# Kernel optimization log

Measured on AMD Instinct MI355X. Metric: run time of the kernel, lower is better.

## Reference

```python
import jax, jax.numpy as jnp
import numpy as np

B, T, C = 2, 512, 128
H = 4 * C
EPS_LN = 1e-5
EPS_WKV = 1e-6


def setup_inputs() -> dict:
    key = jax.random.key(0)
    ks = jax.random.split(key, 12)
    def rn(i, shape, s):
        return jax.random.normal(ks[i], shape, jnp.float32) * s
    return {
        "x": jax.random.normal(ks[0], (B, T, C), jnp.float32),
        "ln1_g": jnp.ones((C,), jnp.float32), "ln1_b": jnp.zeros((C,), jnp.float32),
        "mu": rn(1, (C,), 0.1),
        "Wr": rn(2, (C, C), 0.02), "br": jnp.zeros((C,), jnp.float32),
        "Wk": rn(3, (C, C), 0.02), "bk": jnp.zeros((C,), jnp.float32),
        "Wv": rn(4, (C, C), 0.02), "bv": jnp.zeros((C,), jnp.float32),
        "w_decay": rn(5, (C,), 0.5),
        "Wo": rn(6, (C, C), 0.02), "bo": jnp.zeros((C,), jnp.float32),
        "ln2_g": jnp.ones((C,), jnp.float32), "ln2_b": jnp.zeros((C,), jnp.float32),
        "W1": rn(7, (C, H), 0.02), "b1": jnp.zeros((H,), jnp.float32),
        "W2": rn(8, (H, C), 0.02), "b2": jnp.zeros((C,), jnp.float32),
    }


def _ln(x, g, b):
    m = x.mean(-1, keepdims=True)
    v = ((x - m) ** 2).mean(-1, keepdims=True)
    return (x - m) * jax.lax.rsqrt(v + EPS_LN) * g + b


def _wkv_dir(k, v, w_lc):
    # k, v: (B,T,C); w_lc: (T,C) per-(position,channel) decay weight
    p = k[:, :, None, :] * w_lc[None, None, :, :]              # (B,T,L,C)
    p = jnp.exp(p - jax.lax.stop_gradient(p.max(-1, keepdims=True)))  # stable, max over C (as in source, dim=-1)
    p = p / (p.sum(-1, keepdims=True) + EPS_WKV)               # normalize over channel dim, as written in torch
    return jnp.einsum('btlc,blc->btc', p, v)


def _forward(x, ln1_g, ln1_b, mu, Wr, br, Wk, bk, Wv, bv, w_decay, Wo, bo, ln2_g, ln2_b, W1, b1, W2, b2):
    Tn = x.shape[1]
    h = _ln(x, ln1_g, ln1_b)
    # TemporalShift: past half shifted right, future half shifted left
    xp, xf = jnp.split(h, 2, axis=-1)
    xp = jnp.pad(xp, ((0, 0), (1, 0), (0, 0)))[:, :-1]
    xf = jnp.pad(xf, ((0, 0), (0, 1), (0, 0)))[:, 1:]
    hs = h + mu * jnp.concatenate([xp, xf], axis=-1)
    r = jax.nn.sigmoid(hs @ Wr + br)
    k = hs @ Wk + bk
    v = hs @ Wv + bv
    t = jnp.arange(Tn, dtype=x.dtype)[:, None]                 # (T,1)
    neg_w = -jnp.exp(w_decay)[None, :]                         # (1,C)
    w_f = neg_w * (Tn - 1 - t) / (Tn - 1)                      # (T,C)
    w_b = neg_w * t / (Tn - 1)                                 # (T,C)
    x_f = _wkv_dir(k, v, w_f)
    x_b = jnp.flip(_wkv_dir(jnp.flip(k, 1), jnp.flip(v, 1), w_b), 1)
    wk = r * (x_f + x_b) * 0.5
    y = x + wk @ Wo + bo
    h2 = _ln(y, ln2_g, ln2_b)
    m = jax.nn.gelu(h2 @ W1 + b1, approximate=False) @ W2 + b2
    return y + m


def reference(x, ln1_g, ln1_b, mu, Wr, br, Wk, bk, Wv, bv, w_decay, Wo, bo, ln2_g, ln2_b, W1, b1, W2, b2):
    return _forward(x, ln1_g, ln1_b, mu, Wr, br, Wk, bk, Wv, bv, w_decay, Wo, bo, ln2_g, ln2_b, W1, b1, W2, b2)
```

## Files before the change

kernel.cpp:

```cpp
#include <hip/hip_runtime.h>
#include <hip/hip_bf16.h>

#define Bq 2
#define Tq 512
#define Cq 128
#define Hq 512
#define NROW (Bq*Tq)

__device__ __forceinline__ float bfbits2f(unsigned short u) {
    return __uint_as_float(((unsigned)u) << 16);
}
__device__ __forceinline__ bool detect_f32(const void* sent) {
    return *(const unsigned*)sent == 0x3F800000u;
}
#define LD(p, i) (f32 ? ((const float*)(p))[i] : bfbits2f(((const unsigned short*)(p))[i]))
__device__ __forceinline__ float4 LD4(const void* p, int i, bool f32) {
    if (f32) return ((const float4*)p)[i >> 2];
    ushort4 u = *(const ushort4*)((const unsigned short*)p + i);
    return make_float4(bfbits2f(u.x), bfbits2f(u.y), bfbits2f(u.z), bfbits2f(u.w));
}

__global__ __launch_bounds__(512) void k2_qkv(
    const void* __restrict__ sent,
    const void* __restrict__ x,
    const void* __restrict__ ln1g, const void* __restrict__ ln1b,
    const void* __restrict__ mu,
    const void* __restrict__ Wr, const void* __restrict__ br,
    const void* __restrict__ Wk, const void* __restrict__ bk,
    const void* __restrict__ Wv, const void* __restrict__ bv,
    const void* __restrict__ wdec,
    float* __restrict__ r_out, float* __restrict__ u_out,
    float* __restrict__ v_out)
{
    const bool f32 = detect_f32(sent);
    int R0 = blockIdx.x * 2, tid = threadIdx.x;
    int g = tid >> 7, col = tid & 127;
    int t0 = R0 & (Tq - 1);
    int bbase = R0 - t0;

    __shared__ float h4[4][Cq];
    __shared__ float hs2[2][Cq];
    __shared__ float part[4][6][Cq];
    __shared__ float wred[8][2];

    {
        int t = t0 - 1 + g;
        int tcl = min(max(t, 0), Tq - 1);
        int row = bbase + tcl;
        float xv = LD(x, row * Cq + col);
        float s1 = xv, s2 = xv * xv;
        for (int off = 32; off; off >>= 1) {
            s1 += __shfl_xor(s1, off);
            s2 += __shfl_xor(s2, off);
        }
        int wid = tid >> 6;
        if ((tid & 63) == 0) { wred[wid][0] = s1; wred[wid][1] = s2; }
        __syncthreads();
        float S1 = wred[2 * g][0] + wred[2 * g + 1][0];
        float S2 = wred[2 * g][1] + wred[2 * g + 1][1];
        float m  = S1 * (1.f / Cq);
        float va = S2 * (1.f / Cq) - m * m;
        float rs = rsqrtf(va + 1e-5f);
        h4[g][col] = (xv - m) * rs * LD(ln1g, col) + LD(ln1b, col);
    }
    __syncthreads();

    if (g < 2) {
        int r2 = g, tt = t0 + r2;
        float hv = h4[r2 + 1][col];
        float nb;
        if (col < Cq / 2) nb = (tt > 0)      ? h4[r2][col]     : 0.f;
        else              nb = (tt < Tq - 1) ? h4[r2 + 2][col] : 0.f;
        hs2[r2][col] = hv + LD(mu, col) * nb;
    }
    __syncthreads();

    {
        float ar0 = 0.f, ar1 = 0.f, ak0 = 0.f, ak1 = 0.f, av0 = 0.f, av1 = 0.f;
        int c0 = g * 32;
        for (int cc = c0; cc < c0 + 32; cc += 4) {
            float4 h0 = *(const float4*)&hs2[0][cc];
            float4 h1 = *(const float4*)&hs2[1][cc];
            float wr0 = LD(Wr, (cc + 0) * Cq + col);
            float wr1 = LD(Wr, (cc + 1) * Cq + col);
            float wr2 = LD(Wr, (cc + 2) * Cq + col);
            float wr3 = LD(Wr, (cc + 3) * Cq + col);
            float wk0 = LD(Wk, (cc + 0) * Cq + col);
            float wk1 = LD(Wk, (cc + 1) * Cq + col);
            float wk2 = LD(Wk, (cc + 2) * Cq + col);
            float wk3 = LD(Wk, (cc + 3) * Cq + col);
            float wv0 = LD(Wv, (cc + 0) * Cq + col);
            float wv1 = LD(Wv, (cc + 1) * Cq + col);
            float wv2 = LD(Wv, (cc + 2) * Cq + col);
            float wv3 = LD(Wv, (cc + 3) * Cq + col);
            ar0 += h0.x * wr0; ar1 += h1.x * wr0;
            ak0 += h0.x * wk0; ak1 += h1.x * wk0;
            av0 += h0.x * wv0; av1 += h1.x * wv0;
            ar0 += h0.y * wr1; ar1 += h1.y * wr1;
            ak0 += h0.y * wk1; ak1 += h1.y * wk1;
            av0 += h0.y * wv1; av1 += h1.y * wv1;
            ar0 += h0.z * wr2; ar1 += h1.z * wr2;
            ak0 += h0.z * wk2; ak1 += h1.z * wk2;
            av0 += h0.z * wv2; av1 += h1.z * wv2;
            ar0 += h0.w * wr3; ar1 += h1.w * wr3;
            ak0 += h0.w * wk3; ak1 += h1.w * wk3;
            av0 += h0.w * wv3; av1 += h1.w * wv3;
        }
        part[g][0][col] = ar0; part[g][1][col] = ar1;
        part[g][2][col] = ak0; part[g][3][col] = ak1;
        part[g][4][col] = av0; part[g][5][col] = av1;
    }
    __syncthreads();

    if (g < 3) {
#pragma unroll
        for (int r2 = 0; r2 < 2; ++r2) {
            int m = 2 * g + r2;
            float a = (part[0][m][col] + part[1][m][col])
                    + (part[2][m][col] + part[3][m][col]);
            int row = R0 + r2;
            if (g == 0) {
                float rr = 1.f / (1.f + __expf(-(a + LD(br, col))));
                r_out[row * Cq + col] = rr;
            } else if (g == 1) {
                float wd = LD(wdec, col);
                wd = fminf(fmaxf(wd, -20.f), 20.f);
                float negw = -__expf(wd);
                float uu = (a + LD(bk, col)) * negw;
                uu = fminf(fmaxf(uu, -30.f), 30.f);
                u_out[row * Cq + col] = uu;
            } else {
                v_out[row * Cq + col] = a + LD(bv, col);
            }
        }
    }
}

__global__ __launch_bounds__(512) void k3_wkv(
    const void* __restrict__ sent,
    const float* __restrict__ u_in,
    const float* __restrict__ v_in,
    const float* __restrict__ r_in,
    const void* __restrict__ x,
    const void* __restrict__ Wo, const void* __restrict__ bo,
    float* __restrict__ y_out)
{
    const bool f32 = detect_f32(sent);
    int row = blockIdx.x, tid = threadIdx.x;
    int b = row >> 9;
    __shared__ float u_l[Cq];
    __shared__ float rinv_l[Tq];
    __shared__ float wk_l[Cq];
    __shared__ float part[8][Cq];
    __shared__ float part2[4][Cq];
    if (tid < Cq) u_l[tid] = u_in[row * Cq + tid];
    __syncthreads();

    const float inv511 = 1.f / (float)(Tq - 1);
    {
        int l = tid;
        float a = (float)(Tq - 1 - l) * inv511 * 1.44269504f;
        float s0 = 0.f, s1 = 0.f, s2 = 0.f, s3 = 0.f;
        const float4* u4 = (const float4*)u_l;
        for (int cc = 0; cc < Cq / 4; ++cc) {
            float4 uv = u4[cc];
            s0 += exp2f(a * uv.x);
            s1 += exp2f(a * uv.y);
            s2 += exp2f(a * uv.z);
            s3 += exp2f(a * uv.w);
        }
        rinv_l[l] = 1.f / ((s0 + s1) + (s2 + s3) + 1e-6f);
    }
    __syncthreads();

    {
        int cidx = tid & 63, seg = tid >> 6;
        int c2 = cidx * 2;
        float2 uu = *(const float2*)&u_l[c2];
        float g1x = __expf(uu.x * inv511),      g1y = __expf(uu.y * inv511);
        float g2x = g1x * g1x,                  g2y = g1y * g1y;
        float g3x = g2x * g1x,                  g3y = g2y * g1y;
        float g4x = g2x * g2x,                  g4y = g2y * g2y;
        float jb  = (float)(seg * 64);
        float ex  = __expf(uu.x * jb * inv511), ey = __expf(uu.y * jb * inv511);
        float a0x = 0.f, a0y = 0.f, a1x = 0.f, a1y = 0.f;
        float a2x = 0.f, a2y = 0.f, a3x = 0.f, a3y = 0.f;
        const float2* vb2 = (const float2*)(v_in + (size_t)b * Tq * Cq) + cidx;
        int j0 = seg * 64;
        for (int j = j0; j < j0 + 64; j += 4) {
            int l = (Tq - 1) - j;
            float4 rv = *(const float4*)&rinv_l[l - 3];
            float2 v0 = vb2[(size_t)l * 64];
            float2 v1 = vb2[(size_t)(l - 1) * 64];
            float2 v2 = vb2[(size_t)(l - 2) * 64];
            float2 v3 = vb2[(size_t)(l - 3) * 64];
            a0x += v0.x * (ex * rv.w);          a0y += v0.y * (ey * rv.w);
            a1x += v1.x * ((ex * g1x) * rv.z);  a1y += v1.y * ((ey * g1y) * rv.z);
            a2x += v2.x * ((ex * g2x) * rv.y);  a2y += v2.y * ((ey * g2y) * rv.y);
            a3x += v3.x * ((ex * g3x) * rv.x);  a3y += v3.y * ((ey * g3y) * rv.x);
            ex *= g4x; ey *= g4y;
        }
        float px = (a0x + a1x) + (a2x + a3x);
        float py = (a0y + a1y) + (a2y + a3y);
        *(float2*)&part[seg][c2] = make_float2(px, py);
    }
    __syncthreads();
    if (tid < Cq) {
        float acc = ((part[0][tid] + part[1][tid]) + (part[2][tid] + part[3][tid]))
                  + ((part[4][tid] + part[5][tid]) + (part[6][tid] + part[7][tid]));
        wk_l[tid] = r_in[row * Cq + tid] * acc;
    }
    __syncthreads();

    {
        int seg4 = tid >> 7, c = tid & 127;
        float s = 0.f;
        int c0 = seg4 * 32;
        for (int cc = c0; cc < c0 + 32; cc += 4) {
            float4 wv4 = *(const float4*)&wk_l[cc];
            s += wv4.x * LD(Wo, (cc + 0) * Cq + c);
            s += wv4.y * LD(Wo, (cc + 1) * Cq + c);
            s += wv4.z * LD(Wo, (cc + 2) * Cq + c);
            s += wv4.w * LD(Wo, (cc + 3) * Cq + c);
        }
        part2[seg4][c] = s;
    }
    __syncthreads();
    if (tid < Cq)
        y_out[row * Cq + tid] = LD(x, row * Cq + tid)
            + ((part2[0][tid] + part2[1][tid]) + (part2[2][tid] + part2[3][tid]))
            + LD(bo, tid);
}

__global__ __launch_bounds__(512) void k4_ffn(
    const void* __restrict__ sent,
    const float* __restrict__ y_in,
    const void* __restrict__ lng, const void* __restrict__ lnb,
    const void* __restrict__ W1, const void* __restrict__ b1,
    const void* __restrict__ W2, const void* __restrict__ b2,
    void* __restrict__ out)
{
    const bool f32 = detect_f32(sent);
    int R0 = blockIdx.x * 2, tid = threadIdx.x;
    __shared__ float h2s[2][Cq];
    __shared__ float m1s[2][Hq];
    __shared__ float part1[4][2][Hq];
    __shared__ float part[4][2][Cq];
    __shared__ float wred[8][2];
    int r2 = (tid >> 7) & 1, c = tid & 127;
    float yv = 0.f;
    if (tid < 256) yv = y_in[(R0 + r2) * Cq + c];
    float s1 = yv, s2 = yv * yv;
    for (int off = 32; off; off >>= 1) {
        s1 += __shfl_xor(s1, off);
        s2 += __shfl_xor(s2, off);
    }
    int wid = tid >> 6;
    if ((tid & 63) == 0) { wred[wid][0] = s1; wred[wid][1] = s2; }
    __syncthreads();
    if (tid < 256) {
        int w0 = r2 << 1;
        float S1 = wred[w0][0] + wred[w0 + 1][0];
        float S2 = wred[w0][1] + wred[w0 + 1][1];
        float m  = S1 * (1.f / Cq);
        float va = S2 * (1.f / Cq) - m * m;
        float rs = rsqrtf(va + 1e-5f);
        h2s[r2][c] = (yv - m) * rs * LD(lng, c) + LD(lnb, c);
    }
    __syncthreads();

    {
        int kseg = tid >> 7, j4 = (tid & 127) * 4;
        float a00 = 0.f, a01 = 0.f, a02 = 0.f, a03 = 0.f;
        float a10 = 0.f, a11 = 0.f, a12 = 0.f, a13 = 0.f;
        int c0 = kseg * 32;
        for (int cc = c0; cc < c0 + 32; cc += 4) {
            float4 w0 = LD4(W1, (cc + 0) * Hq + j4, f32);
            float4 w1 = LD4(W1, (cc + 1) * Hq + j4, f32);
            float4 w2 = LD4(W1, (cc + 2) * Hq + j4, f32);
            float4 w3 = LD4(W1, (cc + 3) * Hq + j4, f32);
            float4 h0 = *(const float4*)&h2s[0][cc];
            float4 h1 = *(const float4*)&h2s[1][cc];
            a00 += h0.x * w0.x; a01 += h0.x * w0.y; a02 += h0.x * w0.z; a03 += h0.x * w0.w;
            a10 += h1.x * w0.x; a11 += h1.x * w0.y; a12 += h1.x * w0.z; a13 += h1.x * w0.w;
            a00 += h0.y * w1.x; a01 += h0.y * w1.y; a02 += h0.y * w1.z; a03 += h0.y * w1.w;
            a10 += h1.y * w1.x; a11 += h1.y * w1.y; a12 += h1.y * w1.z; a13 += h1.y * w1.w;
            a00 += h0.z * w2.x; a01 += h0.z * w2.y; a02 += h0.z * w2.z; a03 += h0.z * w2.w;
            a10 += h1.z * w2.x; a11 += h1.z * w2.y; a12 += h1.z * w2.z; a13 += h1.z * w2.w;
            a00 += h0.w * w3.x; a01 += h0.w * w3.y; a02 += h0.w * w3.z; a03 += h0.w * w3.w;
            a10 += h1.w * w3.x; a11 += h1.w * w3.y; a12 += h1.w * w3.z; a13 += h1.w * w3.w;
        }
        *(float4*)&part1[kseg][0][j4] = make_float4(a00, a01, a02, a03);
        *(float4*)&part1[kseg][1][j4] = make_float4(a10, a11, a12, a13);
    }
    __syncthreads();
    {
        int j = tid;
        float bb = LD(b1, j);
        float x0 = ((part1[0][0][j] + part1[1][0][j]) + (part1[2][0][j] + part1[3][0][j])) + bb;
        float x1 = ((part1[0][1][j] + part1[1][1][j]) + (part1[2][1][j] + part1[3][1][j])) + bb;
        m1s[0][j] = 0.5f * x0 * (1.f + erff(x0 * 0.70710678f));
        m1s[1][j] = 0.5f * x1 * (1.f + erff(x1 * 0.70710678f));
    }
    __syncthreads();

    {
        int kseg = tid >> 7;
        int h0 = kseg * 128;
        float a0 = 0.f, a1 = 0.f;
        for (int hh = h0; hh < h0 + 128; hh += 8) {
            float4 ma = *(const float4*)&m1s[0][hh];
            float4 mb = *(const float4*)&m1s[0][hh + 4];
            float4 na = *(const float4*)&m1s[1][hh];
            float4 nb = *(const float4*)&m1s[1][hh + 4];
            float w0 = LD(W2, (hh + 0) * Cq + c);
            float w1 = LD(W2, (hh + 1) * Cq + c);
            float w2 = LD(W2, (hh + 2) * Cq + c);
            float w3 = LD(W2, (hh + 3) * Cq + c);
            float w4 = LD(W2, (hh + 4) * Cq + c);
            float w5 = LD(W2, (hh + 5) * Cq + c);
            float w6 = LD(W2, (hh + 6) * Cq + c);
            float w7 = LD(W2, (hh + 7) * Cq + c);
            a0 += ma.x * w0; a1 += na.x * w0;
            a0 += ma.y * w1; a1 += na.y * w1;
            a0 += ma.z * w2; a1 += na.z * w2;
            a0 += ma.w * w3; a1 += na.w * w3;
            a0 += mb.x * w4; a1 += nb.x * w4;
            a0 += mb.y * w5; a1 += nb.y * w5;
            a0 += mb.z * w6; a1 += nb.z * w6;
            a0 += mb.w * w7; a1 += nb.w * w7;
        }
        part[kseg][0][c] = a0;
        part[kseg][1][c] = a1;
    }
    __syncthreads();
    if (tid < 256) {
        float s = ((part[0][r2][c] + part[1][r2][c]) + (part[2][r2][c] + part[3][r2][c]));
        float val = yv + s + LD(b2, c);
        int idx = (R0 + r2) * Cq + c;
        if (f32) ((float*)out)[idx] = val;
        else     ((__hip_bfloat16*)out)[idx] = __float2bfloat16(val);
    }
}

extern "C" void kernel_launch(void* const* d_in, const int* in_sizes, int n_in,
                              void* d_out, int out_size, void* d_ws, size_t ws_size,
                              hipStream_t stream)
{
    const void* x    = d_in[0];
    const void* ln1g = d_in[1];
    const void* ln1b = d_in[2];
    const void* mu   = d_in[3];
    const void* Wr   = d_in[4];
    const void* br   = d_in[5];
    const void* Wk   = d_in[6];
    const void* bk   = d_in[7];
    const void* Wv   = d_in[8];
    const void* bv   = d_in[9];
    const void* wdec = d_in[10];
    const void* Wo   = d_in[11];
    const void* bo   = d_in[12];
    const void* ln2g = d_in[13];
    const void* ln2b = d_in[14];
    const void* W1   = d_in[15];
    const void* b1   = d_in[16];
    const void* W2   = d_in[17];
    const void* b2   = d_in[18];

    float* ws = (float*)d_ws;
    float* u  = ws;
    float* r  = ws + 131072;
    float* y  = ws + 262144;
    float* v  = ws + 393216;

    k2_qkv<<<NROW / 2, 512, 0, stream>>>(ln1g, x, ln1g, ln1b, mu, Wr, br, Wk, bk, Wv, bv, wdec, r, u, v);
    k3_wkv<<<NROW,     512, 0, stream>>>(ln1g, u, v, r, x, Wo, bo, y);
    k4_ffn<<<NROW / 2, 512, 0, stream>>>(ln1g, y, ln2g, ln2b, W1, b1, W2, b2, d_out);
}
```

Before: 153.8 us.

## Fuse WKV and FFN kernels, process four rows per 1024-thread block with staged V

```diff
diff --git a/kernel.cpp b/kernel.cpp
--- a/kernel.cpp
+++ b/kernel.cpp
@@ -136,208 +136,216 @@
     }
 }
 
-__global__ __launch_bounds__(512) void k3_wkv(
+__global__ __launch_bounds__(1024) void k34_wkv_ffn(
     const void* __restrict__ sent,
     const float* __restrict__ u_in,
     const float* __restrict__ v_in,
     const float* __restrict__ r_in,
     const void* __restrict__ x,
     const void* __restrict__ Wo, const void* __restrict__ bo,
-    float* __restrict__ y_out)
-{
-    const bool f32 = detect_f32(sent);
-    int row = blockIdx.x, tid = threadIdx.x;
-    int b = row >> 9;
-    __shared__ float u_l[Cq];
-    __shared__ float rinv_l[Tq];
-    __shared__ float wk_l[Cq];
-    __shared__ float part[8][Cq];
-    __shared__ float part2[4][Cq];
-    if (tid < Cq) u_l[tid] = u_in[row * Cq + tid];
-    __syncthreads();
-
-    const float inv511 = 1.f / (float)(Tq - 1);
-    {
-        int l = tid;
-        float a = (float)(Tq - 1 - l) * inv511 * 1.44269504f;
-        float s0 = 0.f, s1 = 0.f, s2 = 0.f, s3 = 0.f;
-        const float4* u4 = (const float4*)u_l;
-        for (int cc = 0; cc < Cq / 4; ++cc) {
-            float4 uv = u4[cc];
-            s0 += exp2f(a * uv.x);
-            s1 += exp2f(a * uv.y);
-            s2 += exp2f(a * uv.z);
-            s3 += exp2f(a * uv.w);
-        }
-        rinv_l[l] = 1.f / ((s0 + s1) + (s2 + s3) + 1e-6f);
-    }
-    __syncthreads();
-
-    {
-        int cidx = tid & 63, seg = tid >> 6;
-        int c2 = cidx * 2;
-        float2 uu = *(const float2*)&u_l[c2];
-        float g1x = __expf(uu.x * inv511),      g1y = __expf(uu.y * inv511);
-        float g2x = g1x * g1x,                  g2y = g1y * g1y;
-        float g3x = g2x * g1x,                  g3y = g2y * g1y;
-        float g4x = g2x * g2x,                  g4y = g2y * g2y;
-        float jb  = (float)(seg * 64);
-        float ex  = __expf(uu.x * jb * inv511), ey = __expf(uu.y * jb * inv511);
-        float a0x = 0.f, a0y = 0.f, a1x = 0.f, a1y = 0.f;
-        float a2x = 0.f, a2y = 0.f, a3x = 0.f, a3y = 0.f;
-        const float2* vb2 = (const float2*)(v_in + (size_t)b * Tq * Cq) + cidx;
-        int j0 = seg * 64;
-        for (int j = j0; j < j0 + 64; j += 4) {
-            int l = (Tq - 1) - j;
-            float4 rv = *(const float4*)&rinv_l[l - 3];
-            float2 v0 = vb2[(size_t)l * 64];
-            float2 v1 = vb2[(size_t)(l - 1) * 64];
-            float2 v2 = vb2[(size_t)(l - 2) * 64];
-            float2 v3 = vb2[(size_t)(l - 3) * 64];
-            a0x += v0.x * (ex * rv.w);          a0y += v0.y * (ey * rv.w);
-            a1x += v1.x * ((ex * g1x) * rv.z);  a1y += v1.y * ((ey * g1y) * rv.z);
-            a2x += v2.x * ((ex * g2x) * rv.y);  a2y += v2.y * ((ey * g2y) * rv.y);
-            a3x += v3.x * ((ex * g3x) * rv.x);  a3y += v3.y * ((ey * g3y) * rv.x);
-            ex *= g4x; ey *= g4y;
-        }
-        float px = (a0x + a1x) + (a2x + a3x);
-        float py = (a0y + a1y) + (a2y + a3y);
-        *(float2*)&part[seg][c2] = make_float2(px, py);
-    }
-    __syncthreads();
-    if (tid < Cq) {
-        float acc = ((part[0][tid] + part[1][tid]) + (part[2][tid] + part[3][tid]))
-                  + ((part[4][tid] + part[5][tid]) + (part[6][tid] + part[7][tid]));
-        wk_l[tid] = r_in[row * Cq + tid] * acc;
-    }
-    __syncthreads();
-
-    {
-        int seg4 = tid >> 7, c = tid & 127;
-        float s = 0.f;
-        int c0 = seg4 * 32;
-        for (int cc = c0; cc < c0 + 32; cc += 4) {
-            float4 wv4 = *(const float4*)&wk_l[cc];
-            s += wv4.x * LD(Wo, (cc + 0) * Cq + c);
-            s += wv4.y * LD(Wo, (cc + 1) * Cq + c);
-            s += wv4.z * LD(Wo, (cc + 2) * Cq + c);
-            s += wv4.w * LD(Wo, (cc + 3) * Cq + c);
-        }
-        part2[seg4][c] = s;
-    }
-    __syncthreads();
-    if (tid < Cq)
-        y_out[row * Cq + tid] = LD(x, row * Cq + tid)
-            + ((part2[0][tid] + part2[1][tid]) + (part2[2][tid] + part2[3][tid]))
-            + LD(bo, tid);
-}
-
-__global__ __launch_bounds__(512) void k4_ffn(
-    const void* __restrict__ sent,
-    const float* __restrict__ y_in,
     const void* __restrict__ lng, const void* __restrict__ lnb,
     const void* __restrict__ W1, const void* __restrict__ b1,
     const void* __restrict__ W2, const void* __restrict__ b2,
     void* __restrict__ out)
 {
     const bool f32 = detect_f32(sent);
-    int R0 = blockIdx.x * 2, tid = threadIdx.x;
-    __shared__ float h2s[2][Cq];
-    __shared__ float m1s[2][Hq];
-    __shared__ float part1[4][2][Hq];
-    __shared__ float part[4][2][Cq];
-    __shared__ float wred[8][2];
-    int r2 = (tid >> 7) & 1, c = tid & 127;
-    float yv = 0.f;
-    if (tid < 256) yv = y_in[(R0 + r2) * Cq + c];
-    float s1 = yv, s2 = yv * yv;
-    for (int off = 32; off; off >>= 1) {
-        s1 += __shfl_xor(s1, off);
-        s2 += __shfl_xor(s2, off);
-    }
-    int wid = tid >> 6;
-    if ((tid & 63) == 0) { wred[wid][0] = s1; wred[wid][1] = s2; }
-    __syncthreads();
-    if (tid < 256) {
-        int w0 = r2 << 1;
-        float S1 = wred[w0][0] + wred[w0 + 1][0];
-        float S2 = wred[w0][1] + wred[w0 + 1][1];
-        float m  = S1 * (1.f / Cq);
-        float va = S2 * (1.f / Cq) - m * m;
-        float rs = rsqrtf(va + 1e-5f);
-        h2s[r2][c] = (yv - m) * rs * LD(lng, c) + LD(lnb, c);
-    }
-    __syncthreads();
-
-    {
-        int kseg = tid >> 7, j4 = (tid & 127) * 4;
+    int R0 = blockIdx.x * 4, tid = threadIdx.x;
+    int b = R0 >> 9;
+    const float inv511 = 1.f / (float)(Tq - 1);
+
+    __shared__ float u4[4][Cq];
+    __shared__ float rinv[4][Tq];
+    __shared__ float vbuf[2][32][Cq];
+    __shared__ float pp2[2][4][Cq];
+    __shared__ float wk4[4][Cq];
+    __shared__ float pwo[2][4][Cq];
+    __shared__ float y4[4][Cq];
+    __shared__ float h2s[4][Cq];
+    __shared__ float part1[4][4][Hq];
+    __shared__ float m1s[4][Hq];
+    __shared__ float part2[8][4][Cq];
+    __shared__ float wred[16][2];
+
+    if (tid < 512) {
+        int r = tid >> 7, c = tid & 127;
+        u4[r][c] = u_in[(R0 + r) * Cq + c];
+    }
+    __syncthreads();
+
+    {
+        int l = tid & 511, rb = (tid >> 9) * 2;
+        float a = (float)(Tq - 1 - l) * inv511 * 1.44269504f;
+#pragma unroll
+        for (int rr = rb; rr < rb + 2; ++rr) {
+            float s0 = 0.f, s1 = 0.f, s2 = 0.f, s3 = 0.f;
+            const float4* uu4 = (const float4*)u4[rr];
+            for (int cc = 0; cc < Cq / 4; ++cc) {
+                float4 uv = uu4[cc];
+                s0 += exp2f(a * uv.x);
+                s1 += exp2f(a * uv.y);
+                s2 += exp2f(a * uv.z);
+                s3 += exp2f(a * uv.w);
+            }
+            rinv[rr][l] = 1.f / ((s0 + s1) + (s2 + s3) + 1e-6f);
+        }
+    }
+
+    const float4* v4g = (const float4*)v_in + (size_t)b * (Tq * Cq / 4);
+    ((float4*)vbuf[0])[tid] = v4g[tid];
+    __syncthreads();
+
+    {
+        int r = tid >> 8, h = (tid >> 7) & 1, c = tid & 127;
+        float uu = u4[r][c];
+        float gi1 = __expf(-uu * inv511);
+        float gi2 = gi1 * gi1, gi3 = gi2 * gi1, gi4 = gi2 * gi2;
+        float gi16 = gi4 * gi4; gi16 *= gi16;
+        float gi32 = gi16 * gi16;
+        float el0 = __expf(uu * (float)(Tq - 1 - 16 * h) * inv511);
+        float a0 = 0.f, a1 = 0.f, a2 = 0.f, a3 = 0.f;
+        for (int ci = 0; ci < 16; ++ci) {
+            int cur = ci & 1;
+            float4 vnext;
+            if (ci < 15) vnext = v4g[(ci + 1) * 1024 + tid];
+            int lb = ci * 32 + h * 16;
+            int lloc = h * 16;
+            float el = el0;
+#pragma unroll
+            for (int q = 0; q < 4; ++q) {
+                float4 rv = *(const float4*)&rinv[r][lb + 4 * q];
+                float v0 = vbuf[cur][lloc + 4 * q + 0][c];
+                float v1 = vbuf[cur][lloc + 4 * q + 1][c];
+                float v2 = vbuf[cur][lloc + 4 * q + 2][c];
+                float v3 = vbuf[cur][lloc + 4 * q + 3][c];
+                a0 += v0 * (el * rv.x);
+                a1 += v1 * ((el * gi1) * rv.y);
+                a2 += v2 * ((el * gi2) * rv.z);
+                a3 += v3 * ((el * gi3) * rv.w);
+                el *= gi4;
+            }
+            el0 *= gi32;
+            if (ci < 15) ((float4*)vbuf[cur ^ 1])[tid] = vnext;
+            __syncthreads();
+        }
+        pp2[h][r][c] = (a0 + a1) + (a2 + a3);
+    }
+    __syncthreads();
+
+    if (tid < 512) {
+        int r = tid >> 7, c = tid & 127;
+        float acc = pp2[0][r][c] + pp2[1][r][c];
+        wk4[r][c] = r_in[(R0 + r) * Cq + c] * acc;
+    }
+    __syncthreads();
+
+    {
+        int r = tid >> 8, ks = (tid >> 7) & 1, c = tid & 127;
+        float s = 0.f;
+        int k0 = ks * 64;
+        for (int kk = k0; kk < k0 + 64; kk += 4) {
+            float4 w = *(const float4*)&wk4[r][kk];
+            s += w.x * LD(Wo, (kk + 0) * Cq + c);
+            s += w.y * LD(Wo, (kk + 1) * Cq + c);
+            s += w.z * LD(Wo, (kk + 2) * Cq + c);
+            s += w.w * LD(Wo, (kk + 3) * Cq + c);
+        }
+        pwo[ks][r][c] = s;
+    }
+    __syncthreads();
+    if (tid < 512) {
+        int r = tid >> 7, c = tid & 127;
+        y4[r][c] = LD(x, (R0 + r) * Cq + c) + pwo[0][r][c] + pwo[1][r][c] + LD(bo, c);
+    }
+    __syncthreads();
+
+    {
+        int r = tid >> 7, c = tid & 127;
+        float yv = (tid < 512) ? y4[r][c] : 0.f;
+        float s1 = yv, s2 = yv * yv;
+        for (int off = 32; off; off >>= 1) {
+            s1 += __shfl_xor(s1, off);
+            s2 += __shfl_xor(s2, off);
+        }
+        int wid = tid >> 6;
+        if ((tid & 63) == 0) { wred[wid][0] = s1; wred[wid][1] = s2; }
+        __syncthreads();
+        if (tid < 512) {
+            float S1 = wred[2 * r][0] + wred[2 * r + 1][0];
+            float S2 = wred[2 * r][1] + wred[2 * r + 1][1];
+            float m  = S1 * (1.f / Cq);
+            float va = S2 * (1.f / Cq) - m * m;
+            float rs = rsqrtf(va + 1e-5f);
+            h2s[r][c] = (yv - m) * rs * LD(lng, c) + LD(lnb, c);
+        }
+    }
+    __syncthreads();
+
+    {
+        int ks = (tid >> 7) & 3, rh = tid >> 9, j4 = (tid & 127) * 4;
+        int ra = 2 * rh, rb2 = 2 * rh + 1;
         float a00 = 0.f, a01 = 0.f, a02 = 0.f, a03 = 0.f;
         float a10 = 0.f, a11 = 0.f, a12 = 0.f, a13 = 0.f;
-        int c0 = kseg * 32;
+        int c0 = ks * 32;
         for (int cc = c0; cc < c0 + 32; cc += 4) {
             float4 w0 = LD4(W1, (cc + 0) * Hq + j4, f32);
             float4 w1 = LD4(W1, (cc + 1) * Hq + j4, f32);
             float4 w2 = LD4(W1, (cc + 2) * Hq + j4, f32);
             float4 w3 = LD4(W1, (cc + 3) * Hq + j4, f32);
-            float4 h0 = *(const float4*)&h2s[0][cc];
-            float4 h1 = *(const float4*)&h2s[1][cc];
-            a00 += h0.x * w0.x; a01 += h0.x * w0.y; a02 += h0.x * w0.z; a03 += h0.x * w0.w;
-            a10 += h1.x * w0.x; a11 += h1.x * w0.y; a12 += h1.x * w0.z; a13 += h1.x * w0.w;
-            a00 += h0.y * w1.x; a01 += h0.y * w1.y; a02 += h0.y * w1.z; a03 += h0.y * w1.w;
-            a10 += h1.y * w1.x; a11 += h1.y * w1.y; a12 += h1.y * w1.z; a13 += h1.y * w1.w;
-            a00 += h0.z * w2.x; a01 += h0.z * w2.y; a02 += h0.z * w2.z; a03 += h0.z * w2.w;
-            a10 += h1.z * w2.x; a11 += h1.z * w2.y; a12 += h1.z * w2.z; a13 += h1.z * w2.w;
-            a00 += h0.w * w3.x; a01 += h0.w * w3.y; a02 += h0.w * w3.z; a03 += h0.w * w3.w;
-            a10 += h1.w * w3.x; a11 += h1.w * w3.y; a12 += h1.w * w3.z; a13 += h1.w * w3.w;
-        }
-        *(float4*)&part1[kseg][0][j4] = make_float4(a00, a01, a02, a03);
-        *(float4*)&part1[kseg][1][j4] = make_float4(a10, a11, a12, a13);
-    }
-    __syncthreads();
-    {
-        int j = tid;
+            float4 ha = *(const float4*)&h2s[ra][cc];
+            float4 hb = *(const float4*)&h2s[rb2][cc];
+            a00 += ha.x * w0.x; a01 += ha.x * w0.y; a02 += ha.x * w0.z; a03 += ha.x * w0.w;
+            a10 += hb.x * w0.x; a11 += hb.x * w0.y; a12 += hb.x * w0.z; a13 += hb.x * w0.w;
+            a00 += ha.y * w1.x; a01 += ha.y * w1.y; a02 += ha.y * w1.z; a03 += ha.y * w1.w;
+            a10 += hb.y * w1.x; a11 += hb.y * w1.y; a12 += hb.y * w1.z; a13 += hb.y * w1.w;
+            a00 += ha.z * w2.x; a01 += ha.z * w2.y; a02 += ha.z * w2.z; a03 += ha.z * w2.w;
+            a10 += hb.z * w2.x; a11 += hb.z * w2.y; a12 += hb.z * w2.z; a13 += hb.z * w2.w;
+            a00 += ha.w * w3.x; a01 += ha.w * w3.y; a02 += ha.w * w3.z; a03 += ha.w * w3.w;
+            a10 += hb.w * w3.x; a11 += hb.w * w3.y; a12 += hb.w * w3.z; a13 += hb.w * w3.w;
+        }
+        *(float4*)&part1[ks][ra][j4]  = make_float4(a00, a01, a02, a03);
+        *(float4*)&part1[ks][rb2][j4] = make_float4(a10, a11, a12, a13);
+    }
+    __syncthreads();
+    {
+        int j = tid & 511, rh = tid >> 9;
         float bb = LD(b1, j);
-        float x0 = ((part1[0][0][j] + part1[1][0][j]) + (part1[2][0][j] + part1[3][0][j])) + bb;
-        float x1 = ((part1[0][1][j] + part1[1][1][j]) + (part1[2][1][j] + part1[3][1][j])) + bb;
-        m1s[0][j] = 0.5f * x0 * (1.f + erff(x0 * 0.70710678f));
-        m1s[1][j] = 0.5f * x1 * (1.f + erff(x1 * 0.70710678f));
-    }
-    __syncthreads();
-
-    {
-        int kseg = tid >> 7;
-        int h0 = kseg * 128;
-        float a0 = 0.f, a1 = 0.f;
-        for (int hh = h0; hh < h0 + 128; hh += 8) {
-            float4 ma = *(const float4*)&m1s[0][hh];
-            float4 mb = *(const float4*)&m1s[0][hh + 4];
-            float4 na = *(const float4*)&m1s[1][hh];
-            float4 nb = *(const float4*)&m1s[1][hh + 4];
+#pragma unroll
+        for (int rr = 2 * rh; rr < 2 * rh + 2; ++rr) {
+            float xg = ((part1[0][rr][j] + part1[1][rr][j])
+                      + (part1[2][rr][j] + part1[3][rr][j])) + bb;
+            m1s[rr][j] = 0.5f * xg * (1.f + erff(xg * 0.70710678f));
+        }
+    }
+    __syncthreads();
+
+    {
+        int ks = tid >> 7, c = tid & 127;
+        int h0 = ks * 64;
+        float a0 = 0.f, a1 = 0.f, a2 = 0.f, a3 = 0.f;
+        for (int hh = h0; hh < h0 + 64; hh += 4) {
+            float4 m0 = *(const float4*)&m1s[0][hh];
+            float4 m1v = *(const float4*)&m1s[1][hh];
+            float4 m2 = *(const float4*)&m1s[2][hh];
+            float4 m3 = *(const float4*)&m1s[3][hh];
             float w0 = LD(W2, (hh + 0) * Cq + c);
             float w1 = LD(W2, (hh + 1) * Cq + c);
             float w2 = LD(W2, (hh + 2) * Cq + c);
             float w3 = LD(W2, (hh + 3) * Cq + c);
-            float w4 = LD(W2, (hh + 4) * Cq + c);
-            float w5 = LD(W2, (hh + 5) * Cq + c);
-            float w6 = LD(W2, (hh + 6) * Cq + c);
-            float w7 = LD(W2, (hh + 7) * Cq + c);
-            a0 += ma.x * w0; a1 += na.x * w0;
-            a0 += ma.y * w1; a1 += na.y * w1;
-            a0 += ma.z * w2; a1 += na.z * w2;
-            a0 += ma.w * w3; a1 += na.w * w3;
-            a0 += mb.x * w4; a1 += nb.x * w4;
-            a0 += mb.y * w5; a1 += nb.y * w5;
-            a0 += mb.z * w6; a1 += nb.z * w6;
-            a0 += mb.w * w7; a1 += nb.w * w7;
-        }
-        part[kseg][0][c] = a0;
-        part[kseg][1][c] = a1;
-    }
-    __syncthreads();
-    if (tid < 256) {
-        float s = ((part[0][r2][c] + part[1][r2][c]) + (part[2][r2][c] + part[3][r2][c]));
-        float val = yv + s + LD(b2, c);
-        int idx = (R0 + r2) * Cq + c;
+            a0 += m0.x * w0; a1 += m1v.x * w0; a2 += m2.x * w0; a3 += m3.x * w0;
+            a0 += m0.y * w1; a1 += m1v.y * w1; a2 += m2.y * w1; a3 += m3.y * w1;
+            a0 += m0.z * w2; a1 += m1v.z * w2; a2 += m2.z * w2; a3 += m3.z * w2;
+            a0 += m0.w * w3; a1 += m1v.w * w3; a2 += m2.w * w3; a3 += m3.w * w3;
+        }
+        part2[ks][0][c] = a0; part2[ks][1][c] = a1;
+        part2[ks][2][c] = a2; part2[ks][3][c] = a3;
+    }
+    __syncthreads();
+    if (tid < 512) {
+        int r = tid >> 7, c = tid & 127;
+        float s = ((part2[0][r][c] + part2[1][r][c]) + (part2[2][r][c] + part2[3][r][c]))
+                + ((part2[4][r][c] + part2[5][r][c]) + (part2[6][r][c] + part2[7][r][c]));
+        float val = y4[r][c] + s + LD(b2, c);
+        int idx = (R0 + r) * Cq + c;
         if (f32) ((float*)out)[idx] = val;
         else     ((__hip_bfloat16*)out)[idx] = __float2bfloat16(val);
     }
@@ -370,10 +378,8 @@
     float* ws = (float*)d_ws;
     float* u  = ws;
     float* r  = ws + 131072;
-    float* y  = ws + 262144;
-    float* v  = ws + 393216;
+    float* v  = ws + 262144;
 
     k2_qkv<<<NROW / 2, 512, 0, stream>>>(ln1g, x, ln1g, ln1b, mu, Wr, br, Wk, bk, Wv, bv, wdec, r, u, v);
-    k3_wkv<<<NROW,     512, 0, stream>>>(ln1g, u, v, r, x, Wo, bo, y);
-    k4_ffn<<<NROW / 2, 512, 0, stream>>>(ln1g, y, ln2g, ln2b, W1, b1, W2, b2, d_out);
-}
+    k34_wkv_ffn<<<NROW / 4, 1024, 0, stream>>>(ln1g, u, v, r, x, Wo, bo, ln2g, ln2b, W1, b1, W2, b2, d_out);
+}
```

New measurement: 174.2 us. 13.2% more time.
